# Performance work log

Hardware: AMD Instinct MI355X
Metric: run time of the kernel (lower is better)

The kernel has to match this reference:

```python
import jax, jax.numpy as jnp
import numpy as np

WS = 7          # window size
NH = 12         # num heads
DIM = 384
HID = 4 * DIM
EPS = 1e-5


def _rel_pos_index(ws):
    coords = np.stack(np.meshgrid(np.arange(ws), np.arange(ws), indexing='ij'))  # (2,ws,ws)
    cf = coords.reshape(2, -1)
    rel = cf[:, :, None] - cf[:, None, :]           # (2,N,N)
    rel = rel.transpose(1, 2, 0)                    # (N,N,2)
    rel[:, :, 0] += ws - 1
    rel[:, :, 1] += ws - 1
    rel[:, :, 0] *= 2 * ws - 1
    return jnp.asarray(rel.sum(-1))                 # (N,N) int

REL_IDX = _rel_pos_index(WS)


def _layernorm(x, g, b):
    m = x.mean(-1, keepdims=True)
    v = ((x - m) ** 2).mean(-1, keepdims=True)
    return (x - m) * jax.lax.rsqrt(v + EPS) * g + b


def setup_inputs() -> dict:
    key = jax.random.key(0)
    ks = jax.random.split(key, 16)
    B, H, W = 8, 112, 112
    s = lambda fan: 1.0 / np.sqrt(fan)
    return {
        'x': jax.random.normal(ks[0], (B, DIM, H, W), jnp.float32),
        'g1': jnp.ones((DIM,), jnp.float32),
        'b1': jnp.zeros((DIM,), jnp.float32),
        'w_qkv': jax.random.normal(ks[1], (DIM, 3 * DIM), jnp.float32) * s(DIM),
        'b_qkv': jnp.zeros((3 * DIM,), jnp.float32),
        'rpb': jax.random.normal(ks[2], ((2 * WS - 1) ** 2, NH), jnp.float32) * 0.02,
        'w_proj': jax.random.normal(ks[3], (DIM, DIM), jnp.float32) * s(DIM),
        'b_proj': jnp.zeros((DIM,), jnp.float32),
        'g2': jnp.ones((DIM,), jnp.float32),
        'b2': jnp.zeros((DIM,), jnp.float32),
        'w_fc1': jax.random.normal(ks[4], (DIM, HID), jnp.float32) * s(DIM),
        'b_fc1': jnp.zeros((HID,), jnp.float32),
        'w_fc2': jax.random.normal(ks[5], (HID, DIM), jnp.float32) * s(HID),
        'b_fc2': jnp.zeros((DIM,), jnp.float32),
    }


def reference(x, g1, b1, w_qkv, b_qkv, rpb, w_proj, b_proj, g2, b2, w_fc1, b_fc1, w_fc2, b_fc2):
    B, C, H, W = x.shape
    x = x.transpose(0, 2, 3, 1)                     # (B,H,W,C)
    shortcut = x
    xn = _layernorm(x, g1, b1)

    # window partition (with padding, no-op when divisible)
    pad_h = (-H) % WS
    pad_w = (-W) % WS
    if pad_h or pad_w:
        xn = jnp.pad(xn, ((0, 0), (0, pad_h), (0, pad_w), (0, 0)))
    Hp, Wp = H + pad_h, W + pad_w
    N = WS * WS
    xw = xn.reshape(B, Hp // WS, WS, Wp // WS, WS, C).transpose(0, 1, 3, 2, 4, 5)
    xw = xw.reshape(-1, N, C)                       # (B_, N, C)
    B_ = xw.shape[0]
    hd = C // NH

    qkv = (xw @ w_qkv + b_qkv).reshape(B_, N, 3, NH, hd)
    q = qkv[:, :, 0].transpose(0, 2, 1, 3) * (hd ** -0.5)   # (B_,h,N,d)
    k = qkv[:, :, 1].transpose(0, 2, 1, 3)
    v = qkv[:, :, 2].transpose(0, 2, 1, 3)

    attn = jnp.einsum('bhnd,bhmd->bhnm', q, k)
    bias = rpb[REL_IDX.reshape(-1)].reshape(N, N, NH).transpose(2, 0, 1)  # (h,N,N)
    attn = jax.nn.softmax(attn + bias[None], axis=-1)

    out = jnp.einsum('bhnm,bhmd->bhnd', attn, v).transpose(0, 2, 1, 3).reshape(B_, N, C)
    out = out @ w_proj + b_proj

    # window reverse
    out = out.reshape(B, Hp // WS, Wp // WS, WS, WS, C).transpose(0, 1, 3, 2, 4, 5)
    out = out.reshape(B, Hp, Wp, C)[:, :H, :W]

    x = shortcut + out
    h = _layernorm(x, g2, b2)
    h = jax.nn.gelu(h @ w_fc1 + b_fc1, approximate=False) @ w_fc2 + b_fc2
    x = x + h
    return x.transpose(0, 3, 1, 2)                  # (B,C,H,W)
```

## Files before the change

kernel.cpp:

```cpp
#include <hip/hip_runtime.h>
#include <cstdint>
#include <cmath>

using u16 = unsigned short;

typedef __bf16 bf16x8 __attribute__((ext_vector_type(8)));
typedef float  f32x4  __attribute__((ext_vector_type(4)));

__device__ __forceinline__ float b2f(u16 u) {
    return __uint_as_float(((unsigned int)u) << 16);
}
__device__ __forceinline__ u16 f2b(float f) {
    unsigned int x = __float_as_uint(f);
    unsigned int r = (x + 0x7fffu + ((x >> 16) & 1u)) >> 16;
    return (u16)r;
}

__device__ __forceinline__ void gload16(const u16* g, u16* l) {
    __builtin_amdgcn_global_load_lds((__attribute__((address_space(1))) void*)g,
                                     (__attribute__((address_space(3))) void*)l,
                                     16, 0, 0);
}

__device__ __forceinline__ float gelu_f(float x) {
    float z = fabsf(x) * 0.70710678118f;
    float t = __builtin_amdgcn_rcpf(fmaf(0.3275911f, z, 1.0f));
    float poly = fmaf(fmaf(fmaf(fmaf(1.061405429f, t, -1.453152027f),
                               t, 1.421413741f),
                          t, -0.284496736f),
                     t, 0.254829592f) * t;
    float e = __expf(-z * z);
    float erfv = copysignf(1.0f - poly * e, x);
    return 0.5f * x * (1.0f + erfv);
}

__device__ __forceinline__ int tprime(int b, int hw) {
    int r = hw / 112, c = hw - r * 112;
    int wy = r / 7, iy = r - wy * 7;
    int wx = c / 7, ix = c - wx * 7;
    return (b * 256 + wy * 16 + wx) * 49 + iy * 7 + ix;
}

__global__ void detect_dtype(const unsigned int* __restrict__ x, int* __restrict__ flag) {
    __shared__ int cnt[256];
    int tid = threadIdx.x;
    int c = 0;
#pragma unroll
    for (int i = 0; i < 16; ++i) {
        unsigned int w = x[tid * 16 + i];
        int e = (w >> 23) & 0xFF;
        if (e >= 100 && e <= 150) ++c;
    }
    cnt[tid] = c;
    __syncthreads();
    if (tid == 0) {
        int s = 0;
        for (int i = 0; i < 256; ++i) s += cnt[i];
        flag[0] = (s > 3072) ? 1 : 0;
    }
}

__global__ void convertk(const void* __restrict__ src, u16* __restrict__ dst, int n,
                         const int* __restrict__ flagp) {
    int isf = flagp[0];
    int i = blockIdx.x * 256 + threadIdx.x;
    if (i < n) dst[i] = isf ? f2b(((const float*)src)[i]) : ((const u16*)src)[i];
}

__global__ void wtrans(const u16* __restrict__ in, u16* __restrict__ out, int K, int N) {
    __shared__ u16 tile[32][33];
    int n0 = blockIdx.x * 32, k0 = blockIdx.y * 32;
    int tx = threadIdx.x & 31, ty = threadIdx.x >> 5;
#pragma unroll
    for (int i = 0; i < 4; ++i)
        tile[ty + i * 8][tx] = in[(size_t)(k0 + ty + i * 8) * N + n0 + tx];
    __syncthreads();
#pragma unroll
    for (int i = 0; i < 4; ++i)
        out[(size_t)(n0 + ty + i * 8) * K + k0 + tx] = tile[tx][ty + i * 8];
}

__global__ void ln1_stats(const void* __restrict__ x, float* __restrict__ mean,
                          float* __restrict__ rstd, const int* __restrict__ flagp) {
    int isf = flagp[0];
    int t = blockIdx.x * 256 + threadIdx.x;
    int b = t / 12544, hw = t - b * 12544;
    size_t base = (size_t)b * 384 * 12544 + hw;
    float s = 0.f, sq = 0.f;
    if (isf) {
        const float* p = (const float*)x + base;
        for (int c = 0; c < 384; ++c) {
            float v = p[(size_t)c * 12544];
            s += v; sq += v * v;
        }
    } else {
        const u16* p = (const u16*)x + base;
        for (int c = 0; c < 384; ++c) {
            float v = b2f(p[(size_t)c * 12544]);
            s += v; sq += v * v;
        }
    }
    float m = s * (1.0f / 384.0f);
    float var = sq * (1.0f / 384.0f) - m * m;
    mean[t] = m;
    rstd[t] = rsqrtf(var + 1e-5f);
}

__global__ void ln1_apply(const void* __restrict__ x, const float* __restrict__ mean,
                          const float* __restrict__ rstd, const u16* __restrict__ g1,
                          const u16* __restrict__ b1, u16* __restrict__ xt,
                          u16* __restrict__ xn, const int* __restrict__ flagp) {
    __shared__ float tile[64][65];
    int isf = flagp[0];
    int hw0 = blockIdx.x * 64, c0 = blockIdx.y * 64, b = blockIdx.z;
    int tid = threadIdx.x;
    {
        int hl = tid & 63, cq = tid >> 6;
        size_t base = ((size_t)b * 384 + c0) * 12544 + hw0;
#pragma unroll
        for (int it = 0; it < 16; ++it) {
            int cl = cq * 16 + it;
            size_t idx = base + (size_t)cl * 12544 + hl;
            tile[cl][hl] = isf ? ((const float*)x)[idx] : b2f(((const u16*)x)[idx]);
        }
    }
    __syncthreads();
    {
        int cl = tid & 63, hq = tid >> 6;
        float g = b2f(g1[c0 + cl]), bb = b2f(b1[c0 + cl]);
#pragma unroll
        for (int it = 0; it < 16; ++it) {
            int hl = hq * 16 + it;
            int hw = hw0 + hl;
            int t = b * 12544 + hw;
            int tp = tprime(b, hw);
            float v = tile[cl][hl];
            size_t o = (size_t)tp * 384 + c0 + cl;
            xt[o] = f2b(v);
            xn[o] = f2b((v - mean[t]) * rstd[t] * g + bb);
        }
    }
}

template <int EPI>
__global__ void gemm_bt(const u16* __restrict__ A, const u16* __restrict__ Bt,
                        const u16* __restrict__ bias, const u16* __restrict__ res,
                        u16* __restrict__ Cout, int M, int N, int K) {
    __shared__ __align__(16) u16 S[2][2][128 * 32];
    const int tid = threadIdx.x;
    const int wave = tid >> 6, lane = tid & 63;

    const int nbx = gridDim.x;
    const int nwg = nbx * gridDim.y;
    int flat = blockIdx.y * nbx + blockIdx.x;
    {
        int q = nwg >> 3, r = nwg & 7;
        int xcd = flat & 7, loc = flat >> 3;
        flat = (xcd < r ? xcd * (q + 1) : r * (q + 1) + (xcd - r) * q) + loc;
    }
    const int m0 = (flat / nbx) * 128, n0 = (flat % nbx) * 128;

    const int wm = wave & 1, wn = wave >> 1;
    const int m15 = lane & 15, q4 = lane >> 4;

    const u16* gA = A + (size_t)(m0 + wave * 32 + (lane >> 2)) * K + (lane & 3) * 8;
    const u16* gB = Bt + (size_t)(n0 + wave * 32 + (lane >> 2)) * K + (lane & 3) * 8;

    f32x4 acc[4][4];
#pragma unroll
    for (int i = 0; i < 4; ++i)
#pragma unroll
        for (int j = 0; j < 4; ++j) acc[i][j] = {0.f, 0.f, 0.f, 0.f};

    const int nt = K >> 5;
    {
        u16* lA = &S[0][0][(wave * 32) * 32];
        u16* lB = &S[0][1][(wave * 32) * 32];
        gload16(gA, lA);
        gload16(gA + 16 * (size_t)K, lA + 16 * 32);
        gload16(gB, lB);
        gload16(gB + 16 * (size_t)K, lB + 16 * 32);
    }
    __syncthreads();

    for (int t = 0; t < nt; ++t) {
        const int cur = t & 1;
        if (t + 1 < nt) {
            const int k0 = (t + 1) << 5;
            u16* lA = &S[cur ^ 1][0][(wave * 32) * 32];
            u16* lB = &S[cur ^ 1][1][(wave * 32) * 32];
            gload16(gA + k0, lA);
            gload16(gA + k0 + 16 * (size_t)K, lA + 16 * 32);
            gload16(gB + k0, lB);
            gload16(gB + k0 + 16 * (size_t)K, lB + 16 * 32);
        }
        bf16x8 af[4], bfr[4];
#pragma unroll
        for (int i = 0; i < 4; ++i)
            af[i] = *(const bf16x8*)&S[cur][0][(wm * 64 + i * 16 + m15) * 32 + q4 * 8];
#pragma unroll
        for (int j = 0; j < 4; ++j)
            bfr[j] = *(const bf16x8*)&S[cur][1][(wn * 64 + j * 16 + m15) * 32 + q4 * 8];
#pragma unroll
        for (int i = 0; i < 4; ++i)
#pragma unroll
            for (int j = 0; j < 4; ++j)
                acc[i][j] = __builtin_amdgcn_mfma_f32_16x16x32_bf16(af[i], bfr[j],
                                                                    acc[i][j], 0, 0, 0);
        __syncthreads();
    }

    constexpr int CSTR = 132;
    float* Cs = (float*)&S[0][0][0];
#pragma unroll
    for (int p = 0; p < 4; ++p) {
        __syncthreads();
        if (wm == (p >> 1)) {
            const int ibase = (p & 1) * 2;
#pragma unroll
            for (int jj = 0; jj < 4; ++jj) {
                int n = n0 + wn * 64 + jj * 16 + m15;
                float bv = b2f(bias[n]);
#pragma unroll
                for (int ii = 0; ii < 2; ++ii) {
                    int i = ibase + ii;
#pragma unroll
                    for (int r = 0; r < 4; ++r) {
                        float v = acc[i][jj][r] + bv;
                        if (EPI == 1) v = gelu_f(v);
                        Cs[(ii * 16 + q4 * 4 + r) * CSTR + wn * 64 + jj * 16 + m15] = v;
                    }
                }
            }
        }
        __syncthreads();
#pragma unroll
        for (int it = 0; it < 2; ++it) {
            int r2 = it * 16 + (tid >> 4);
            int c8 = (tid & 15) * 8;
            size_t goff = (size_t)(m0 + p * 32 + r2) * N + n0 + c8;
            f32x4 v0 = *(const f32x4*)&Cs[r2 * CSTR + c8];
            f32x4 v1 = *(const f32x4*)&Cs[r2 * CSTR + c8 + 4];
            uint4 rv = {0u, 0u, 0u, 0u};
            const u16* rp = (const u16*)&rv;
            if (EPI == 2) rv = *(const uint4*)&res[goff];
            u16 outv[8];
#pragma unroll
            for (int e = 0; e < 4; ++e) {
                float a = v0[e];
                if (EPI == 2) a += b2f(rp[e]);
                outv[e] = f2b(a);
                float bq = v1[e];
                if (EPI == 2) bq += b2f(rp[4 + e]);
                outv[4 + e] = f2b(bq);
            }
            *(uint4*)&Cout[goff] = *(const uint4*)outv;
        }
    }
}

__global__ void attn_win(const u16* __restrict__ qkv, const u16* __restrict__ rpb,
                         u16* __restrict__ outp) {
    __shared__ __align__(16) u16 lds[4][6144];
    const int tid = threadIdx.x;
    const int wave = tid >> 6, lane = tid & 63;
    const int t0p = blockIdx.x * 49;
    u16* Qs = &lds[wave][0];
    u16* Ks = &lds[wave][2048];
    u16* Vt = &lds[wave][4096];
    u16* Ps = Qs;
    const int m15 = lane & 15, q4 = lane >> 4;
    const int rr = lane >> 2, dq = lane & 3;
    const float scale = 0.17677669529663687f;

    for (int hl = 0; hl < 3; ++hl) {
        const int h = hl * 4 + wave;
        __syncthreads();
#pragma unroll
        for (int p = 0; p < 4; ++p) {
            int n = p * 16 + rr;
            int nc = n < 49 ? n : 48;
            const u16* gq = qkv + (size_t)(t0p + nc) * 1152 + h * 32 + dq * 8;
            gload16(gq, &Qs[p * 512]);
            gload16(gq + 384, &Ks[p * 512]);
            uint4 vv = {0u, 0u, 0u, 0u};
            if (n < 49) vv = *(const uint4*)(gq + 768);
            const u16* pv = (const u16*)&vv;
#pragma unroll
            for (int ii = 0; ii < 8; ++ii) Vt[(dq * 8 + ii) * 64 + n] = pv[ii];
        }
        __syncthreads();
        bf16x8 qf[4], kf[4];
#pragma unroll
        for (int i = 0; i < 4; ++i)
            qf[i] = *(const bf16x8*)&Qs[(i * 16 + m15) * 32 + q4 * 8];
#pragma unroll
        for (int j = 0; j < 4; ++j)
            kf[j] = *(const bf16x8*)&Ks[(j * 16 + m15) * 32 + q4 * 8];
        bf16x8 vf[2][2];
#pragma unroll
        for (int j = 0; j < 2; ++j)
#pragma unroll
            for (int kk = 0; kk < 2; ++kk)
                vf[j][kk] = *(const bf16x8*)&Vt[(j * 16 + m15) * 64 + kk * 32 + q4 * 8];
        f32x4 sc[4][4];
#pragma unroll
        for (int i = 0; i < 4; ++i)
#pragma unroll
            for (int j = 0; j < 4; ++j) {
                sc[i][j] = {0.f, 0.f, 0.f, 0.f};
                sc[i][j] = __builtin_amdgcn_mfma_f32_16x16x32_bf16(qf[i], kf[j],
                                                                   sc[i][j], 0, 0, 0);
            }
#pragma unroll
        for (int i = 0; i < 4; ++i) {
#pragma unroll
            for (int r = 0; r < 4; ++r) {
                int row = i * 16 + q4 * 4 + r;
                int rc = row < 49 ? row : 48;
                int ri = rc / 7, rj = rc - ri * 7;
#pragma unroll
                for (int j = 0; j < 4; ++j) {
                    int col = j * 16 + m15;
                    int cc = col < 49 ? col : 48;
                    int mi = cc / 7, mj = cc - mi * 7;
                    int idx = ((ri - mi + 6) * 13 + (rj - mj + 6)) * 12 + h;
                    float bias = b2f(rpb[idx]);
                    float s = sc[i][j][r] * scale + bias;
                    sc[i][j][r] = (row < 49 && col < 49) ? s : -1e30f;
                }
            }
        }
#pragma unroll
        for (int i = 0; i < 4; ++i) {
#pragma unroll
            for (int r = 0; r < 4; ++r) {
                float mx = fmaxf(fmaxf(sc[i][0][r], sc[i][1][r]),
                                 fmaxf(sc[i][2][r], sc[i][3][r]));
                mx = fmaxf(mx, __shfl_xor(mx, 1));
                mx = fmaxf(mx, __shfl_xor(mx, 2));
                mx = fmaxf(mx, __shfl_xor(mx, 4));
                mx = fmaxf(mx, __shfl_xor(mx, 8));
                float e0 = __expf(sc[i][0][r] - mx);
                float e1 = __expf(sc[i][1][r] - mx);
                float e2 = __expf(sc[i][2][r] - mx);
                float e3 = __expf(sc[i][3][r] - mx);
                float sum = e0 + e1 + e2 + e3;
                sum += __shfl_xor(sum, 1);
                sum += __shfl_xor(sum, 2);
                sum += __shfl_xor(sum, 4);
                sum += __shfl_xor(sum, 8);
                float inv = 1.0f / sum;
                sc[i][0][r] = e0 * inv;
                sc[i][1][r] = e1 * inv;
                sc[i][2][r] = e2 * inv;
                sc[i][3][r] = e3 * inv;
            }
        }
#pragma unroll
        for (int i = 0; i < 4; ++i)
#pragma unroll
            for (int r = 0; r < 4; ++r)
#pragma unroll
                for (int j = 0; j < 4; ++j)
                    Ps[(i * 16 + q4 * 4 + r) * 64 + j * 16 + m15] = f2b(sc[i][j][r]);
        __syncthreads();
        f32x4 oacc[4][2];
#pragma unroll
        for (int i = 0; i < 4; ++i)
#pragma unroll
            for (int j = 0; j < 2; ++j) oacc[i][j] = {0.f, 0.f, 0.f, 0.f};
#pragma unroll
        for (int i = 0; i < 4; ++i) {
#pragma unroll
            for (int kk = 0; kk < 2; ++kk) {
                bf16x8 pf = *(const bf16x8*)&Ps[(i * 16 + m15) * 64 + kk * 32 + q4 * 8];
#pragma unroll
                for (int j = 0; j < 2; ++j)
                    oacc[i][j] = __builtin_amdgcn_mfma_f32_16x16x32_bf16(pf, vf[j][kk],
                                                                         oacc[i][j], 0, 0, 0);
            }
        }
#pragma unroll
        for (int i = 0; i < 4; ++i) {
#pragma unroll
            for (int r = 0; r < 4; ++r) {
                int row = i * 16 + q4 * 4 + r;
                if (row < 49) {
#pragma unroll
                    for (int j = 0; j < 2; ++j)
                        outp[(size_t)(t0p + row) * 384 + h * 32 + j * 16 + m15] =
                            f2b(oacc[i][j][r]);
                }
            }
        }
    }
}

__global__ void ln2_kernel(const u16* __restrict__ y, const u16* __restrict__ g2,
                           const u16* __restrict__ b2, u16* __restrict__ out) {
    int wave = threadIdx.x >> 6, lane = threadIdx.x & 63;
    size_t t = (size_t)blockIdx.x * 4 + wave;
    const u16* row = y + t * 384;
    float v[6];
    float s = 0.f, sq = 0.f;
#pragma unroll
    for (int i = 0; i < 6; ++i) {
        v[i] = b2f(row[lane + i * 64]);
        s += v[i]; sq += v[i] * v[i];
    }
#pragma unroll
    for (int m = 1; m < 64; m <<= 1) {
        s += __shfl_xor(s, m);
        sq += __shfl_xor(sq, m);
    }
    float mean = s * (1.0f / 384.0f);
    float var = sq * (1.0f / 384.0f) - mean * mean;
    float rstd = rsqrtf(var + 1e-5f);
#pragma unroll
    for (int i = 0; i < 6; ++i) {
        int c = lane + i * 64;
        out[t * 384 + c] = f2b((v[i] - mean) * rstd * b2f(g2[c]) + b2f(b2[c]));
    }
}

__global__ void out_transpose(const u16* __restrict__ fin, void* __restrict__ out,
                              const int* __restrict__ flagp) {
    __shared__ float tile[64][65];
    int isf = flagp[0];
    int hw0 = blockIdx.x * 64, c0 = blockIdx.y * 64, b = blockIdx.z;
    int tid = threadIdx.x;
    {
        int cl = tid & 63, hq = tid >> 6;
#pragma unroll
        for (int it = 0; it < 16; ++it) {
            int hl = hq * 16 + it;
            int tp = tprime(b, hw0 + hl);
            tile[hl][cl] = b2f(fin[(size_t)tp * 384 + c0 + cl]);
        }
    }
    __syncthreads();
    {
        int hl = tid & 63, cq = tid >> 6;
#pragma unroll
        for (int it = 0; it < 16; ++it) {
            int cl = cq * 16 + it;
            size_t o = ((size_t)b * 384 + c0 + cl) * 12544 + hw0 + hl;
            float v = tile[hl][cl];
            if (isf) ((float*)out)[o] = v;
            else     ((u16*)out)[o] = f2b(v);
        }
    }
}

extern "C" void kernel_launch(void* const* d_in, const int* in_sizes, int n_in,
                              void* d_out, int out_size, void* d_ws, size_t ws_size,
                              hipStream_t stream) {
    constexpr int T = 100352, C = 384, HID = 1536, NQ = 1152;
    const void* x      = d_in[0];
    u16* out_any = (u16*)d_out;
    (void)out_any;

    char* ws = (char*)d_ws;
    size_t off = 0;
    auto alloc = [&](size_t bytes) { char* p = ws + off; off += (bytes + 255) & ~(size_t)255; return p; };
    int*   flag   = (int*)alloc(4);
    u16* cw_qkv  = (u16*)alloc((size_t)C * NQ * 2);
    u16* cb_qkv  = (u16*)alloc((size_t)NQ * 2);
    u16* crpb    = (u16*)alloc((size_t)169 * 12 * 2);
    u16* cw_proj = (u16*)alloc((size_t)C * C * 2);
    u16* cb_proj = (u16*)alloc((size_t)C * 2);
    u16* cg1     = (u16*)alloc((size_t)C * 2);
    u16* cb1     = (u16*)alloc((size_t)C * 2);
    u16* cg2     = (u16*)alloc((size_t)C * 2);
    u16* cb2     = (u16*)alloc((size_t)C * 2);
    u16* cw_fc1  = (u16*)alloc((size_t)C * HID * 2);
    u16* cb_fc1  = (u16*)alloc((size_t)HID * 2);
    u16* cw_fc2  = (u16*)alloc((size_t)HID * C * 2);
    u16* cb_fc2  = (u16*)alloc((size_t)C * 2);
    u16* wqkvT  = (u16*)alloc((size_t)C * NQ * 2);
    u16* wprojT = (u16*)alloc((size_t)C * C * 2);
    u16* wfc1T  = (u16*)alloc((size_t)C * HID * 2);
    u16* wfc2T  = (u16*)alloc((size_t)HID * C * 2);
    u16*   xt     = (u16*)alloc((size_t)T * C * 2);
    u16*   bufB   = (u16*)alloc((size_t)T * C * 2);
    u16*   bufC   = (u16*)alloc((size_t)T * HID * 2);
    u16*   ybuf   = (u16*)alloc((size_t)T * C * 2);
    float* meanb  = (float*)alloc((size_t)T * 4);
    float* rstdb  = (float*)alloc((size_t)T * 4);

    detect_dtype<<<1, 256, 0, stream>>>((const unsigned int*)x, flag);

    auto conv = [&](const void* src, u16* dst, int n) {
        convertk<<<(n + 255) / 256, 256, 0, stream>>>(src, dst, n, flag);
    };
    conv(d_in[1], cg1, C);
    conv(d_in[2], cb1, C);
    conv(d_in[3], cw_qkv, C * NQ);
    conv(d_in[4], cb_qkv, NQ);
    conv(d_in[5], crpb, 169 * 12);
    conv(d_in[6], cw_proj, C * C);
    conv(d_in[7], cb_proj, C);
    conv(d_in[8], cg2, C);
    conv(d_in[9], cb2, C);
    conv(d_in[10], cw_fc1, C * HID);
    conv(d_in[11], cb_fc1, HID);
    conv(d_in[12], cw_fc2, HID * C);
    conv(d_in[13], cb_fc2, C);

    wtrans<<<dim3(NQ / 32, C / 32), 256, 0, stream>>>(cw_qkv, wqkvT, C, NQ);
    wtrans<<<dim3(C / 32, C / 32), 256, 0, stream>>>(cw_proj, wprojT, C, C);
    wtrans<<<dim3(HID / 32, C / 32), 256, 0, stream>>>(cw_fc1, wfc1T, C, HID);
    wtrans<<<dim3(C / 32, HID / 32), 256, 0, stream>>>(cw_fc2, wfc2T, HID, C);

    ln1_stats<<<T / 256, 256, 0, stream>>>(x, meanb, rstdb, flag);
    ln1_apply<<<dim3(196, 6, 8), 256, 0, stream>>>(x, meanb, rstdb, cg1, cb1, xt, bufB, flag);

    gemm_bt<0><<<dim3(NQ / 128, T / 128), 256, 0, stream>>>(bufB, wqkvT, cb_qkv, nullptr,
                                                            bufC, T, NQ, C);
    attn_win<<<2048, 256, 0, stream>>>(bufC, crpb, bufB);

    gemm_bt<2><<<dim3(C / 128, T / 128), 256, 0, stream>>>(bufB, wprojT, cb_proj, xt,
                                                           ybuf, T, C, C);
    ln2_kernel<<<T / 4, 256, 0, stream>>>(ybuf, cg2, cb2, bufB);

    gemm_bt<1><<<dim3(HID / 128, T / 128), 256, 0, stream>>>(bufB, wfc1T, cb_fc1, nullptr,
                                                             bufC, T, HID, C);
    gemm_bt<2><<<dim3(C / 128, T / 128), 256, 0, stream>>>(bufC, wfc2T, cb_fc2, ybuf,
                                                           bufB, T, C, HID);
    out_transpose<<<dim3(196, 6, 8), 256, 0, stream>>>(bufB, d_out, flag);
}
```

Before: 1.335 ms.

## Load window Q/K straight to registers and drop block barriers in attention

The window-attention kernel now loads the Q and K fragments directly from global memory into registers instead of staging them through LDS. Each wave's LDS region is private, so the block-wide __syncthreads are replaced by a per-wave lgkmcnt wait plus a scheduling barrier. The LDS footprint shrinks and launch bounds are added to allow more resident blocks. Output is staged through LDS so each row is written with 16-byte coalesced stores instead of scattered 2-byte stores. The trade-offs are less coalesced global Q/K loads and reliance on in-order LDS access within a wave for the aliased Vt/P/O buffers.

```diff
diff --git a/kernel.cpp b/kernel.cpp
--- a/kernel.cpp
+++ b/kernel.cpp
@@ -21,6 +21,10 @@
                                      (__attribute__((address_space(3))) void*)l,
                                      16, 0, 0);
 }
+
+#define LGKM0_FENCE() do { \
+    asm volatile("s_waitcnt lgkmcnt(0)" ::: "memory"); \
+    __builtin_amdgcn_sched_barrier(0); } while (0)
 
 __device__ __forceinline__ float gelu_f(float x) {
     float z = fabsf(x) * 0.70710678118f;
@@ -259,44 +263,43 @@
     }
 }
 
-__global__ void attn_win(const u16* __restrict__ qkv, const u16* __restrict__ rpb,
-                         u16* __restrict__ outp) {
-    __shared__ __align__(16) u16 lds[4][6144];
+__global__ __launch_bounds__(256, 4)
+void attn_win(const u16* __restrict__ qkv, const u16* __restrict__ rpb,
+              u16* __restrict__ outp) {
+    __shared__ __align__(16) u16 lds[4][4096];
     const int tid = threadIdx.x;
     const int wave = tid >> 6, lane = tid & 63;
     const int t0p = blockIdx.x * 49;
-    u16* Qs = &lds[wave][0];
-    u16* Ks = &lds[wave][2048];
-    u16* Vt = &lds[wave][4096];
-    u16* Ps = Qs;
+    u16* Vt = &lds[wave][0];
+    u16* Ps = &lds[wave][0];
+    u16* Po = &lds[wave][0];
     const int m15 = lane & 15, q4 = lane >> 4;
     const int rr = lane >> 2, dq = lane & 3;
     const float scale = 0.17677669529663687f;
 
     for (int hl = 0; hl < 3; ++hl) {
         const int h = hl * 4 + wave;
-        __syncthreads();
+        const u16* qbase = qkv + (size_t)t0p * 1152 + h * 32;
+        bf16x8 qf[4], kf[4];
+#pragma unroll
+        for (int i = 0; i < 4; ++i) {
+            int row = i * 16 + m15;
+            int rc = row < 49 ? row : 48;
+            const u16* g = qbase + (size_t)rc * 1152 + q4 * 8;
+            qf[i] = *(const bf16x8*)g;
+            kf[i] = *(const bf16x8*)(g + 384);
+        }
 #pragma unroll
         for (int p = 0; p < 4; ++p) {
             int n = p * 16 + rr;
-            int nc = n < 49 ? n : 48;
-            const u16* gq = qkv + (size_t)(t0p + nc) * 1152 + h * 32 + dq * 8;
-            gload16(gq, &Qs[p * 512]);
-            gload16(gq + 384, &Ks[p * 512]);
             uint4 vv = {0u, 0u, 0u, 0u};
-            if (n < 49) vv = *(const uint4*)(gq + 768);
+            if (n < 49)
+                vv = *(const uint4*)(qbase + (size_t)n * 1152 + 768 + dq * 8);
             const u16* pv = (const u16*)&vv;
 #pragma unroll
             for (int ii = 0; ii < 8; ++ii) Vt[(dq * 8 + ii) * 64 + n] = pv[ii];
         }
-        __syncthreads();
-        bf16x8 qf[4], kf[4];
-#pragma unroll
-        for (int i = 0; i < 4; ++i)
-            qf[i] = *(const bf16x8*)&Qs[(i * 16 + m15) * 32 + q4 * 8];
-#pragma unroll
-        for (int j = 0; j < 4; ++j)
-            kf[j] = *(const bf16x8*)&Ks[(j * 16 + m15) * 32 + q4 * 8];
+        LGKM0_FENCE();
         bf16x8 vf[2][2];
 #pragma unroll
         for (int j = 0; j < 2; ++j)
@@ -364,7 +367,7 @@
 #pragma unroll
                 for (int j = 0; j < 4; ++j)
                     Ps[(i * 16 + q4 * 4 + r) * 64 + j * 16 + m15] = f2b(sc[i][j][r]);
-        __syncthreads();
+        LGKM0_FENCE();
         f32x4 oacc[4][2];
 #pragma unroll
         for (int i = 0; i < 4; ++i)
@@ -382,16 +385,21 @@
             }
         }
 #pragma unroll
-        for (int i = 0; i < 4; ++i) {
+        for (int i = 0; i < 4; ++i)
 #pragma unroll
             for (int r = 0; r < 4; ++r) {
                 int row = i * 16 + q4 * 4 + r;
-                if (row < 49) {
-#pragma unroll
-                    for (int j = 0; j < 2; ++j)
-                        outp[(size_t)(t0p + row) * 384 + h * 32 + j * 16 + m15] =
-                            f2b(oacc[i][j][r]);
-                }
+#pragma unroll
+                for (int j = 0; j < 2; ++j)
+                    Po[row * 40 + j * 16 + m15] = f2b(oacc[i][j][r]);
+            }
+        LGKM0_FENCE();
+#pragma unroll
+        for (int w2 = 0; w2 < 4; ++w2) {
+            int row = w2 * 16 + rr;
+            if (row < 49) {
+                uint4 ov = *(const uint4*)&Po[row * 40 + dq * 8];
+                *(uint4*)&outp[(size_t)(t0p + row) * 384 + h * 32 + dq * 8] = ov;
             }
         }
     }
```

After: 1.338 ms. About the same (+0.2%).
